# Kernel tuning notes

Measured on AMD Instinct MI355X. Metric: run time of the kernel, lower is better.

## Reference

```python
import jax, jax.numpy as jnp
import numpy as np

N = 50000
E = 800000
D = 64
H = 128


def setup_inputs() -> dict:
    key = jax.random.key(0)
    ks = jax.random.split(key, 8)
    x1 = jax.random.normal(ks[0], (N, D), dtype=jnp.float32)
    x2 = jax.random.normal(ks[1], (N, D), dtype=jnp.float32)
    edge_index1 = jax.random.randint(ks[2], (2, E), 0, N, dtype=jnp.int32)
    edge_index2 = jax.random.randint(ks[3], (2, E), 0, N, dtype=jnp.int32)
    W1 = jax.random.normal(ks[4], (2 * D, H), dtype=jnp.float32) * (1.0 / np.sqrt(2 * D))
    b1 = jnp.zeros((H,), dtype=jnp.float32)
    W2 = jax.random.normal(ks[5], (H, D), dtype=jnp.float32) * (1.0 / np.sqrt(H))
    b2 = jnp.zeros((D,), dtype=jnp.float32)
    return {"x1": x1, "x2": x2, "edge_index1": edge_index1, "edge_index2": edge_index2,
            "W1": W1, "b1": b1, "W2": W2, "b2": b2}


def _mlp(e, W1, b1, W2, b2):
    # edge MLP: Linear -> ReLU -> Linear
    h = jax.nn.relu(e @ W1 + b1)
    return h @ W2 + b2


def _scatter_max(vals, row, dim_size):
    # scatter-max aggregation; empty segments (which pyg scatter_ fills with 0)
    out = jax.ops.segment_max(vals, row, num_segments=dim_size)
    return jnp.where(jnp.isfinite(out), out, 0.0)


def reference(x1, x2, edge_index1, edge_index2, W1, b1, W2, b2):
    row1, col1 = edge_index1[0], edge_index1[1]
    # edge features from x1 -> x1: [E, 2D]
    e1 = jnp.concatenate([x1[row1], x1[col1] - x1[row1]], axis=1)
    out1 = _scatter_max(_mlp(e1, W1, b1, W2, b2), row1, x1.shape[0])

    row2, col2 = edge_index2[0], edge_index2[1]
    # edge features from x1 -> x2: [E, 2D]
    e2 = jnp.concatenate([x1[row2], x2[col2] - x1[row2]], axis=1)
    out2 = _scatter_max(_mlp(e2, W1, b1, W2, b2), row2, x2.shape[0])

    return jnp.concatenate([out1, out2], axis=-1)  # [N, 2*D]
```

## Files before the change

### kernel.cpp

```cpp
#include <hip/hip_runtime.h>
#include <hip/hip_bf16.h>

#define NN 50000
#define EE 800000
#define NTILES 12500
#define BPG 512

typedef __attribute__((ext_vector_type(8))) short bf16x8;
typedef __attribute__((ext_vector_type(4))) float f32x4;
typedef __attribute__((ext_vector_type(4))) unsigned u32x4;

__device__ __forceinline__ unsigned enc(float f) {
    unsigned u = __float_as_uint(f);
    return u ^ (unsigned)(((int)u >> 31) | 0x80000000);
}
__device__ __forceinline__ float dec(unsigned u) {
    unsigned v = (u & 0x80000000u) ? (u & 0x7FFFFFFFu) : ~u;
    return __uint_as_float(v);
}
__device__ __forceinline__ unsigned short f2bf(float f) {
    unsigned u = __float_as_uint(f);
    u += 0x7fffu + ((u >> 16) & 1u);
    return (unsigned short)(u >> 16);
}
__device__ __forceinline__ unsigned pk2(float a, float b) {
    __hip_bfloat162 t = __float22bfloat162_rn(make_float2(a, b));
    unsigned r;
    __builtin_memcpy(&r, &t, 4);
    return r;
}

__global__ void init_acc(unsigned* __restrict__ acc, int n) {
    int i = blockIdx.x * blockDim.x + threadIdx.x;
    if (i < n) acc[i] = 0u;
}

__global__ void decode_acc(unsigned* __restrict__ acc, int n) {
    int i = blockIdx.x * blockDim.x + threadIdx.x;
    if (i < n) {
        unsigned u = acc[i];
        ((float*)acc)[i] = (u == 0u) ? 0.0f : dec(u);
    }
}

__global__ __launch_bounds__(256, 2)
void edge_mlp(const float* __restrict__ x1, const float* __restrict__ x2,
              const int* __restrict__ ei1, const int* __restrict__ ei2,
              const float* __restrict__ W1, const float* __restrict__ b1,
              const float* __restrict__ W2, const float* __restrict__ b2,
              unsigned* __restrict__ acc)
{
    __shared__ short e_lds[64 * 128];
    __shared__ short h_lds[64 * 128];
    __shared__ int   srow[2][64];

    const int tid  = threadIdx.x;
    const int lane = tid & 63;
    const int l15  = lane & 15;
    const int lg   = lane >> 4;
    const int wid  = tid >> 6;
    const int w_h  = wid & 1;
    const int w_e  = wid >> 1;

    const int g     = (blockIdx.x >= BPG) ? 1 : 0;
    const int bslot = blockIdx.x & (BPG - 1);
    const int* __restrict__ ei = g ? ei2 : ei1;
    const float* __restrict__ xc = g ? x2 : x1;
    const int goff = g * 64;

    bf16x8 a1[4][4];
    #pragma unroll
    for (int m = 0; m < 4; ++m)
        #pragma unroll
        for (int s = 0; s < 4; ++s) {
            const float* p = W1 + (size_t)(32 * s + 8 * lg) * 128
                               + (w_h * 64 + 16 * m + l15);
            bf16x8 r;
            #pragma unroll
            for (int i = 0; i < 8; ++i) r[i] = (short)f2bf(p[i * 128]);
            a1[m][s] = r;
        }
    bf16x8 b2f[4][2];
    #pragma unroll
    for (int s = 0; s < 4; ++s)
        #pragma unroll
        for (int n = 0; n < 2; ++n) {
            const float* p = W2 + (size_t)(32 * s + 8 * lg) * 64
                               + (w_h * 32 + 16 * n + l15);
            bf16x8 r;
            #pragma unroll
            for (int i = 0; i < 8; ++i) r[i] = (short)f2bf(p[i * 64]);
            b2f[s][n] = r;
        }
    float4 b1v[4];
    #pragma unroll
    for (int m = 0; m < 4; ++m)
        b1v[m] = *(const float4*)(b1 + w_h * 64 + 16 * m + 4 * lg);
    float b2v[2];
    #pragma unroll
    for (int n = 0; n < 2; ++n) b2v[n] = b2[w_h * 32 + 16 * n + l15];

    const int ge = lane;
    const int gq = wid;
    const int swz = (ge & 15) << 3;

    int rcur, ccur, rnext, cnext;
    {
        int ta = bslot;
        rcur = ei[ta * 64 + ge];
        ccur = ei[EE + ta * 64 + ge];
        int tb = ta + BPG; if (tb >= NTILES) tb = NTILES - 1;
        rnext = ei[tb * 64 + ge];
        cnext = ei[EE + tb * 64 + ge];
    }
    float4 gp0, gp1, gp2, gp3, gq0, gq1, gq2, gq3;
    {
        const float4* pp = (const float4*)(x1 + (size_t)rcur * 64 + 16 * gq);
        const float4* pq = (const float4*)(xc + (size_t)ccur * 64 + 16 * gq);
        gp0 = pp[0]; gp1 = pp[1]; gp2 = pp[2]; gp3 = pp[3];
        gq0 = pq[0]; gq1 = pq[1]; gq2 = pq[2]; gq3 = pq[3];
    }

    int i = 0;
    for (int t = bslot; t < NTILES; t += BPG, ++i) {
        if (tid < 64) srow[i & 1][tid] = rcur;
        {
            short* erow = &e_lds[ge * 128];
            u32x4 v;
            v[0] = pk2(gp0.x, gp0.y); v[1] = pk2(gp0.z, gp0.w);
            v[2] = pk2(gp1.x, gp1.y); v[3] = pk2(gp1.z, gp1.w);
            *(u32x4*)&erow[(16 * gq) ^ swz] = v;
            v[0] = pk2(gp2.x, gp2.y); v[1] = pk2(gp2.z, gp2.w);
            v[2] = pk2(gp3.x, gp3.y); v[3] = pk2(gp3.z, gp3.w);
            *(u32x4*)&erow[(16 * gq + 8) ^ swz] = v;
            v[0] = pk2(gq0.x - gp0.x, gq0.y - gp0.y);
            v[1] = pk2(gq0.z - gp0.z, gq0.w - gp0.w);
            v[2] = pk2(gq1.x - gp1.x, gq1.y - gp1.y);
            v[3] = pk2(gq1.z - gp1.z, gq1.w - gp1.w);
            *(u32x4*)&erow[(64 + 16 * gq) ^ swz] = v;
            v[0] = pk2(gq2.x - gp2.x, gq2.y - gp2.y);
            v[1] = pk2(gq2.z - gp2.z, gq2.w - gp2.w);
            v[2] = pk2(gq3.x - gp3.x, gq3.y - gp3.y);
            v[3] = pk2(gq3.z - gp3.z, gq3.w - gp3.w);
            *(u32x4*)&erow[(64 + 16 * gq + 8) ^ swz] = v;
        }

        rcur = rnext; ccur = cnext;
        {
            int t2 = t + 2 * BPG; if (t2 >= NTILES) t2 = NTILES - 1;
            rnext = ei[t2 * 64 + ge];
            cnext = ei[EE + t2 * 64 + ge];
        }
        if (t + BPG < NTILES) {
            const float4* pp = (const float4*)(x1 + (size_t)rcur * 64 + 16 * gq);
            const float4* pq = (const float4*)(xc + (size_t)ccur * 64 + 16 * gq);
            gp0 = pp[0]; gp1 = pp[1]; gp2 = pp[2]; gp3 = pp[3];
            gq0 = pq[0]; gq1 = pq[1]; gq2 = pq[2]; gq3 = pq[3];
        }

        asm volatile("s_waitcnt lgkmcnt(0)\n\ts_barrier" ::: "memory");

        f32x4 acc1[4][2];
        #pragma unroll
        for (int m = 0; m < 4; ++m)
            #pragma unroll
            for (int n = 0; n < 2; ++n) {
                acc1[m][n][0] = b1v[m].x; acc1[m][n][1] = b1v[m].y;
                acc1[m][n][2] = b1v[m].z; acc1[m][n][3] = b1v[m].w;
            }
        __builtin_amdgcn_s_setprio(1);
        #pragma unroll
        for (int s = 0; s < 4; ++s) {
            bf16x8 eb[2];
            #pragma unroll
            for (int n = 0; n < 2; ++n) {
                int e = w_e * 32 + 16 * n + l15;
                int sidx = e * 128 + ((32 * s + 8 * lg) ^ ((e & 15) << 3));
                eb[n] = *(const bf16x8*)&e_lds[sidx];
            }
            #pragma unroll
            for (int m = 0; m < 4; ++m)
                #pragma unroll
                for (int n = 0; n < 2; ++n)
                    acc1[m][n] = __builtin_amdgcn_mfma_f32_16x16x32_bf16(
                        a1[m][s], eb[n], acc1[m][n], 0, 0, 0);
        }
        __builtin_amdgcn_s_setprio(0);
        #pragma unroll
        for (int m = 0; m < 4; ++m)
            #pragma unroll
            for (int n = 0; n < 2; ++n) {
                f32x4 vv = acc1[m][n];
                int e = w_e * 32 + 16 * n + l15;
                int hidc = w_h * 64 + 16 * m + 4 * lg;
                int sidx = e * 128 + (hidc ^ ((e & 15) << 3));
                uint2 w;
                w.x = pk2(fmaxf(vv[0], 0.f), fmaxf(vv[1], 0.f));
                w.y = pk2(fmaxf(vv[2], 0.f), fmaxf(vv[3], 0.f));
                *(uint2*)&h_lds[sidx] = w;
            }

        asm volatile("s_waitcnt lgkmcnt(0)\n\ts_barrier" ::: "memory");

        f32x4 acc2[2][2];
        #pragma unroll
        for (int m = 0; m < 2; ++m)
            #pragma unroll
            for (int n = 0; n < 2; ++n) {
                acc2[m][n][0] = b2v[n]; acc2[m][n][1] = b2v[n];
                acc2[m][n][2] = b2v[n]; acc2[m][n][3] = b2v[n];
            }
        __builtin_amdgcn_s_setprio(1);
        #pragma unroll
        for (int s = 0; s < 4; ++s) {
            bf16x8 ha[2];
            #pragma unroll
            for (int m = 0; m < 2; ++m) {
                int e = w_e * 32 + 16 * m + l15;
                int sidx = e * 128 + ((32 * s + 8 * lg) ^ ((e & 15) << 3));
                ha[m] = *(const bf16x8*)&h_lds[sidx];
            }
            #pragma unroll
            for (int m = 0; m < 2; ++m)
                #pragma unroll
                for (int n = 0; n < 2; ++n)
                    acc2[m][n] = __builtin_amdgcn_mfma_f32_16x16x32_bf16(
                        ha[m], b2f[s][n], acc2[m][n], 0, 0, 0);
        }
        __builtin_amdgcn_s_setprio(0);
        #pragma unroll
        for (int m = 0; m < 2; ++m) {
            int4 rows = *(const int4*)&srow[i & 1][w_e * 32 + 16 * m + 4 * lg];
            #pragma unroll
            for (int n = 0; n < 2; ++n) {
                int outc = w_h * 32 + 16 * n + l15;
                atomicMax(&acc[(size_t)rows.x * 128 + goff + outc], enc(acc2[m][n][0]));
                atomicMax(&acc[(size_t)rows.y * 128 + goff + outc], enc(acc2[m][n][1]));
                atomicMax(&acc[(size_t)rows.z * 128 + goff + outc], enc(acc2[m][n][2]));
                atomicMax(&acc[(size_t)rows.w * 128 + goff + outc], enc(acc2[m][n][3]));
            }
        }
    }
}

extern "C" void kernel_launch(void* const* d_in, const int* in_sizes, int n_in,
                              void* d_out, int out_size, void* d_ws, size_t ws_size,
                              hipStream_t stream) {
    const float* x1 = (const float*)d_in[0];
    const float* x2 = (const float*)d_in[1];
    const int*   ei1 = (const int*)d_in[2];
    const int*   ei2 = (const int*)d_in[3];
    const float* W1 = (const float*)d_in[4];
    const float* b1 = (const float*)d_in[5];
    const float* W2 = (const float*)d_in[6];
    const float* b2 = (const float*)d_in[7];
    unsigned* acc = (unsigned*)d_out;

    const int total = NN * 128;
    hipLaunchKernelGGL(init_acc, dim3((total + 255) / 256), dim3(256), 0, stream,
                       acc, total);
    hipLaunchKernelGGL(edge_mlp, dim3(2 * BPG), dim3(256), 0, stream,
                       x1, x2, ei1, ei2, W1, b1, W2, b2, acc);
    hipLaunchKernelGGL(decode_acc, dim3((total + 255) / 256), dim3(256), 0, stream,
                       acc, total);
}
```

Measured before the change: 305.3 us.

## Sort edges by destination row and pre-reduce scatter-max in shared memory

Adds a counting sort of both edge lists by row (histogram, single-block scan, atomic scatter) so each block processes contiguous sorted tiles. Within each 64-edge tile, edges with the same row are reduced through LDS atomicMax, and only one global atomic per unique row and channel is issued. This targets global atomic traffic and contention in the scatter-max, and improves locality of x1[row] gathers. In exchange it adds three preprocessing kernels and extra workspace traffic, plus more LDS use and barriers per tile inside the MLP kernel.

```diff
diff --git a/kernel.cpp b/kernel.cpp
--- a/kernel.cpp
+++ b/kernel.cpp
@@ -4,7 +4,8 @@
 #define NN 50000
 #define EE 800000
 #define NTILES 12500
-#define BPG 512
+#define BPG 384
+#define TPB_TILES 33
 
 typedef __attribute__((ext_vector_type(8))) short bf16x8;
 typedef __attribute__((ext_vector_type(4))) float f32x4;
@@ -30,11 +31,6 @@
     return r;
 }
 
-__global__ void init_acc(unsigned* __restrict__ acc, int n) {
-    int i = blockIdx.x * blockDim.x + threadIdx.x;
-    if (i < n) acc[i] = 0u;
-}
-
 __global__ void decode_acc(unsigned* __restrict__ acc, int n) {
     int i = blockIdx.x * blockDim.x + threadIdx.x;
     if (i < n) {
@@ -43,16 +39,87 @@
     }
 }
 
+__global__ void hist_k(const int* __restrict__ ei1, const int* __restrict__ ei2,
+                       unsigned* __restrict__ cnt1, unsigned* __restrict__ cnt2) {
+    int idx = blockIdx.x * blockDim.x + threadIdx.x;
+    if (idx < EE)            atomicAdd(&cnt1[ei1[idx]], 1u);
+    else if (idx < 2 * EE)   atomicAdd(&cnt2[ei2[idx - EE]], 1u);
+}
+
+__global__ __launch_bounds__(1024)
+void scan_k(const unsigned* __restrict__ cnt1, const unsigned* __restrict__ cnt2,
+            unsigned* __restrict__ off1, unsigned* __restrict__ off2,
+            unsigned* __restrict__ cur1, unsigned* __restrict__ cur2) {
+    const unsigned* cnt = blockIdx.x ? cnt2 : cnt1;
+    unsigned* off = blockIdx.x ? off2 : off1;
+    unsigned* cur = blockIdx.x ? cur2 : cur1;
+    __shared__ unsigned wsum[16];
+    __shared__ unsigned carry_s;
+    const int tid = threadIdx.x, lane = tid & 63, w = tid >> 6;
+    if (tid == 0) carry_s = 0;
+    __syncthreads();
+    for (int base = 0; base < NN; base += 1024) {
+        int i = base + tid;
+        unsigned x = (i < NN) ? cnt[i] : 0u;
+        unsigned v = x;
+        #pragma unroll
+        for (int o = 1; o < 64; o <<= 1) {
+            unsigned t = __shfl_up(v, o, 64);
+            if (lane >= o) v += t;
+        }
+        if (lane == 63) wsum[w] = v;
+        __syncthreads();
+        if (w == 0) {
+            unsigned s = (lane < 16) ? wsum[lane] : 0u;
+            #pragma unroll
+            for (int o = 1; o < 16; o <<= 1) {
+                unsigned t = __shfl_up(s, o, 64);
+                if (lane >= o) s += t;
+            }
+            if (lane < 16) wsum[lane] = s;
+        }
+        __syncthreads();
+        unsigned wpre = (w > 0) ? wsum[w - 1] : 0u;
+        unsigned carry = carry_s;
+        unsigned excl = carry + wpre + v - x;
+        if (i < NN) { off[i] = excl; cur[i] = excl; }
+        __syncthreads();
+        if (tid == 1023) carry_s = carry + wsum[15];
+        __syncthreads();
+    }
+    if (tid == 0) off[NN] = EE;
+}
+
+__global__ void scatter_k(const int* __restrict__ ei1, const int* __restrict__ ei2,
+                          unsigned* __restrict__ cur1, unsigned* __restrict__ cur2,
+                          int* __restrict__ sr1, int* __restrict__ sc1,
+                          int* __restrict__ sr2, int* __restrict__ sc2) {
+    int idx = blockIdx.x * blockDim.x + threadIdx.x;
+    if (idx < EE) {
+        int r = ei1[idx], c = ei1[EE + idx];
+        unsigned p = atomicAdd(&cur1[r], 1u);
+        sr1[p] = r; sc1[p] = c;
+    } else if (idx < 2 * EE) {
+        int e = idx - EE;
+        int r = ei2[e], c = ei2[EE + e];
+        unsigned p = atomicAdd(&cur2[r], 1u);
+        sr2[p] = r; sc2[p] = c;
+    }
+}
+
 __global__ __launch_bounds__(256, 2)
 void edge_mlp(const float* __restrict__ x1, const float* __restrict__ x2,
-              const int* __restrict__ ei1, const int* __restrict__ ei2,
+              const int* __restrict__ sr1, const int* __restrict__ sc1,
+              const int* __restrict__ sr2, const int* __restrict__ sc2,
               const float* __restrict__ W1, const float* __restrict__ b1,
               const float* __restrict__ W2, const float* __restrict__ b2,
               unsigned* __restrict__ acc)
 {
     __shared__ short e_lds[64 * 128];
     __shared__ short h_lds[64 * 128];
-    __shared__ int   srow[2][64];
+    __shared__ unsigned red[64 * 64];
+    __shared__ int srow[2][64];
+    __shared__ int sslot[2][64];
 
     const int tid  = threadIdx.x;
     const int lane = tid & 63;
@@ -63,10 +130,17 @@
     const int w_e  = wid >> 1;
 
     const int g     = (blockIdx.x >= BPG) ? 1 : 0;
-    const int bslot = blockIdx.x & (BPG - 1);
-    const int* __restrict__ ei = g ? ei2 : ei1;
+    const int bslot = g ? (blockIdx.x - BPG) : blockIdx.x;
+    const int* __restrict__ srw = g ? sr2 : sr1;
+    const int* __restrict__ scl = g ? sc2 : sc1;
     const float* __restrict__ xc = g ? x2 : x1;
     const int goff = g * 64;
+
+    const int t0 = bslot * TPB_TILES;
+    if (t0 >= NTILES) return;
+    const int t1 = min(t0 + TPB_TILES, NTILES);
+
+    for (int k = tid; k < 4096; k += 256) red[k] = 0u;
 
     bf16x8 a1[4][4];
     #pragma unroll
@@ -106,12 +180,11 @@
 
     int rcur, ccur, rnext, cnext;
     {
-        int ta = bslot;
-        rcur = ei[ta * 64 + ge];
-        ccur = ei[EE + ta * 64 + ge];
-        int tb = ta + BPG; if (tb >= NTILES) tb = NTILES - 1;
-        rnext = ei[tb * 64 + ge];
-        cnext = ei[EE + tb * 64 + ge];
+        rcur = srw[t0 * 64 + ge];
+        ccur = scl[t0 * 64 + ge];
+        int tb = min(t0 + 1, t1 - 1);
+        rnext = srw[tb * 64 + ge];
+        cnext = scl[tb * 64 + ge];
     }
     float4 gp0, gp1, gp2, gp3, gq0, gq1, gq2, gq3;
     {
@@ -122,8 +195,9 @@
     }
 
     int i = 0;
-    for (int t = bslot; t < NTILES; t += BPG, ++i) {
-        if (tid < 64) srow[i & 1][tid] = rcur;
+    for (int t = t0; t < t1; ++t, ++i) {
+        const int ib = i & 1;
+        if (tid < 64) srow[ib][tid] = rcur;
         {
             short* erow = &e_lds[ge * 128];
             u32x4 v;
@@ -144,14 +218,22 @@
             v[3] = pk2(gq3.z - gp3.z, gq3.w - gp3.w);
             *(u32x4*)&erow[(64 + 16 * gq + 8) ^ swz] = v;
         }
+        asm volatile("s_waitcnt lgkmcnt(0)" ::: "memory");
+        if (tid < 64) {
+            int r = rcur, lo = 0;
+            #pragma unroll
+            for (int st = 32; st > 0; st >>= 1)
+                if (srow[ib][lo + st - 1] < r) lo += st;
+            sslot[ib][tid] = lo;
+        }
 
         rcur = rnext; ccur = cnext;
         {
-            int t2 = t + 2 * BPG; if (t2 >= NTILES) t2 = NTILES - 1;
-            rnext = ei[t2 * 64 + ge];
-            cnext = ei[EE + t2 * 64 + ge];
-        }
-        if (t + BPG < NTILES) {
+            int t2 = min(t + 2, t1 - 1);
+            rnext = srw[t2 * 64 + ge];
+            cnext = scl[t2 * 64 + ge];
+        }
+        if (t + 1 < t1) {
             const float4* pp = (const float4*)(x1 + (size_t)rcur * 64 + 16 * gq);
             const float4* pq = (const float4*)(xc + (size_t)ccur * 64 + 16 * gq);
             gp0 = pp[0]; gp1 = pp[1]; gp2 = pp[2]; gp3 = pp[3];
@@ -228,16 +310,34 @@
                         ha[m], b2f[s][n], acc2[m][n], 0, 0, 0);
         }
         __builtin_amdgcn_s_setprio(0);
-        #pragma unroll
-        for (int m = 0; m < 2; ++m) {
-            int4 rows = *(const int4*)&srow[i & 1][w_e * 32 + 16 * m + 4 * lg];
-            #pragma unroll
-            for (int n = 0; n < 2; ++n) {
-                int outc = w_h * 32 + 16 * n + l15;
-                atomicMax(&acc[(size_t)rows.x * 128 + goff + outc], enc(acc2[m][n][0]));
-                atomicMax(&acc[(size_t)rows.y * 128 + goff + outc], enc(acc2[m][n][1]));
-                atomicMax(&acc[(size_t)rows.z * 128 + goff + outc], enc(acc2[m][n][2]));
-                atomicMax(&acc[(size_t)rows.w * 128 + goff + outc], enc(acc2[m][n][3]));
+
+        #pragma unroll
+        for (int m = 0; m < 2; ++m)
+            #pragma unroll
+            for (int n = 0; n < 2; ++n) {
+                int ch = w_h * 32 + 16 * n + l15;
+                #pragma unroll
+                for (int r = 0; r < 4; ++r) {
+                    int e_loc = w_e * 32 + 16 * m + 4 * lg + r;
+                    atomicMax(&red[sslot[ib][e_loc] * 64 + ch],
+                              enc(acc2[m][n][r]));
+                }
+            }
+
+        asm volatile("s_waitcnt lgkmcnt(0)\n\ts_barrier" ::: "memory");
+
+        {
+            int e = tid >> 2, q = tid & 3;
+            if (sslot[ib][e] == e) {
+                unsigned rowg = (unsigned)srow[ib][e];
+                unsigned* gdst = acc + (size_t)rowg * 128 + goff + q * 16;
+                unsigned* rsrc = &red[e * 64 + q * 16];
+                #pragma unroll
+                for (int j = 0; j < 16; ++j) {
+                    unsigned u = rsrc[j];
+                    rsrc[j] = 0u;
+                    if (u) atomicMax(&gdst[j], u);
+                }
             }
         }
     }
@@ -256,11 +356,30 @@
     const float* b2 = (const float*)d_in[7];
     unsigned* acc = (unsigned*)d_out;
 
+    unsigned* w = (unsigned*)d_ws;
+    unsigned* cnt1 = w;
+    unsigned* cnt2 = w + 50000;
+    unsigned* off1 = w + 100000;
+    unsigned* off2 = w + 150002;
+    unsigned* cur1 = w + 200004;
+    unsigned* cur2 = w + 250004;
+    int* sr1 = (int*)(w + 300008);
+    int* sc1 = (int*)(w + 1100008);
+    int* sr2 = (int*)(w + 1900008);
+    int* sc2 = (int*)(w + 2700008);
+
+    hipMemsetAsync(cnt1, 0, 100000 * sizeof(unsigned), stream);
+    hipLaunchKernelGGL(hist_k, dim3((2 * EE + 255) / 256), dim3(256), 0, stream,
+                       ei1, ei2, cnt1, cnt2);
+    hipLaunchKernelGGL(scan_k, dim3(2), dim3(1024), 0, stream,
+                       cnt1, cnt2, off1, off2, cur1, cur2);
+    hipLaunchKernelGGL(scatter_k, dim3((2 * EE + 255) / 256), dim3(256), 0, stream,
+                       ei1, ei2, cur1, cur2, sr1, sc1, sr2, sc2);
+
     const int total = NN * 128;
-    hipLaunchKernelGGL(init_acc, dim3((total + 255) / 256), dim3(256), 0, stream,
-                       acc, total);
+    hipMemsetAsync(acc, 0, (size_t)total * sizeof(unsigned), stream);
     hipLaunchKernelGGL(edge_mlp, dim3(2 * BPG), dim3(256), 0, stream,
-                       x1, x2, ei1, ei2, W1, b1, W2, b2, acc);
+                       x1, x2, sr1, sc1, sr2, sc2, W1, b1, W2, b2, acc);
     hipLaunchKernelGGL(decode_acc, dim3((total + 255) / 256), dim3(256), 0, stream,
                        acc, total);
 }
```

Measured after the change: 746.0 us. +144.3%, slower.
